# Kernel tuning notes

Measured on AMD Instinct MI355X. Metric: run time of the kernel, lower is better.

Reference implementation:

```python
import jax, jax.numpy as jnp
import numpy as np

N, E = 4096, 131072
IN, HID, OUT = 128, 128, 256
H4, C4 = 4, HID            # first/middle GAT: 4 heads of 128 -> concat 512
CAT = H4 * C4              # 512
NH, DK = 8, OUT // 8       # dense MHA
EPS_LN = 1e-5


def setup_inputs() -> dict:
    key = jax.random.key(0)
    ks = jax.random.split(key, 32)
    s = 0.05
    inp = {
        "x": jax.random.normal(ks[0], (N, IN), jnp.float32),
        "edge_index": jax.random.randint(ks[1], (2, E), 0, N, jnp.int64),
        # GAT layer 0: in=128, heads=4, out=128
        "W0": jax.random.normal(ks[2], (IN, H4 * C4)) * s,
        "as0": jax.random.normal(ks[3], (H4, C4)) * s,
        "ad0": jax.random.normal(ks[4], (H4, C4)) * s,
        "b0": jnp.zeros((H4 * C4,)),
        # GAT layer 1: in=512, heads=4, out=128
        "W1": jax.random.normal(ks[5], (CAT, H4 * C4)) * s,
        "as1": jax.random.normal(ks[6], (H4, C4)) * s,
        "ad1": jax.random.normal(ks[7], (H4, C4)) * s,
        "b1": jnp.zeros((H4 * C4,)),
        # GAT layer 2: in=512, heads=1, out=256
        "W2": jax.random.normal(ks[8], (CAT, OUT)) * s,
        "as2": jax.random.normal(ks[9], (1, OUT)) * s,
        "ad2": jax.random.normal(ks[10], (1, OUT)) * s,
        "b2": jnp.zeros((OUT,)),
        # LayerNorms
        "g0": jnp.ones((CAT,)), "be0": jnp.zeros((CAT,)),
        "g1": jnp.ones((CAT,)), "be1": jnp.zeros((CAT,)),
        "g2": jnp.ones((OUT,)), "be2": jnp.zeros((OUT,)),
        # dense MHA on output_dim=256
        "wq": jax.random.normal(ks[11], (OUT, OUT)) * s, "bq": jnp.zeros((OUT,)),
        "wk": jax.random.normal(ks[12], (OUT, OUT)) * s, "bk": jnp.zeros((OUT,)),
        "wv": jax.random.normal(ks[13], (OUT, OUT)) * s, "bv": jnp.zeros((OUT,)),
        "wo": jax.random.normal(ks[14], (OUT, OUT)) * s, "bo": jnp.zeros((OUT,)),
    }
    return inp


def _layer_norm(x, g, b):
    mu = x.mean(-1, keepdims=True)
    var = ((x - mu) ** 2).mean(-1, keepdims=True)
    return (x - mu) * jax.lax.rsqrt(var + EPS_LN) * g + b


def _gat(x, src, dst, W, a_src, a_dst, bias, heads, out_c):
    # PyG GATConv (concat=True, negative_slope=0.2, self-loops pre-added)
    n = x.shape[0]
    xl = (x @ W).reshape(n, heads, out_c)            # [N,H,C]
    al_s = (xl * a_src).sum(-1)                      # [N,H]
    al_d = (xl * a_dst).sum(-1)                      # [N,H]
    alpha = jax.nn.leaky_relu(al_s[src] + al_d[dst], 0.2)  # [Etot,H]
    m = jax.ops.segment_max(alpha, dst, num_segments=n)
    e = jnp.exp(alpha - m[dst])
    denom = jax.ops.segment_sum(e, dst, num_segments=n)
    w = e / (denom[dst] + 1e-16)                     # [Etot,H]
    msg = w[:, :, None] * xl[src]                    # [Etot,H,C]
    out = jax.ops.segment_sum(msg, dst, num_segments=n)
    return out.reshape(n, heads * out_c) + bias


def _mha(x, wq, bq, wk, bk, wv, bv, wo, bo):
    # x: [1,N,D], 8 heads
    B, S, D = x.shape
    def split(y):
        return y.reshape(B, S, NH, DK).transpose(0, 2, 1, 3)
    Q, K, V = split(x @ wq + bq), split(x @ wk + bk), split(x @ wv + bv)
    scores = jnp.einsum('bhqd,bhkd->bhqk', Q, K) / np.sqrt(DK)
    attn = jax.nn.softmax(scores, axis=-1)
    out = jnp.einsum('bhqk,bhkd->bhqd', attn, V)
    out = out.transpose(0, 2, 1, 3).reshape(B, S, D)
    return out @ wo + bo


def reference(x, edge_index, W0, as0, ad0, b0, W1, as1, ad1, b1, W2, as2, ad2, b2,
              g0, be0, g1, be1, g2, be2, wq, bq, wk, bk, wv, bv, wo, bo):
    n = x.shape[0]
    loops = jnp.arange(n, dtype=edge_index.dtype)
    src = jnp.concatenate([edge_index[0], loops])
    dst = jnp.concatenate([edge_index[1], loops])

    # layer 0: in=128 -> 512; residual None (128 != 512)
    h = jax.nn.elu(_gat(x, src, dst, W0, as0, ad0, b0, H4, C4))
    h = _layer_norm(h, g0, be0)

    # layer 1: 512 -> 512; residual applies
    res = h
    h = jax.nn.elu(_gat(h, src, dst, W1, as1, ad1, b1, H4, C4))
    h = _layer_norm(h, g1, be1)
    h = h + res

    # layer 2: 512 -> 256, 1 head
    h = _gat(h, src, dst, W2, as2, ad2, b2, 1, OUT)
    h = _layer_norm(h, g2, be2)

    # dense self-attention over all nodes as one sequence
    h = _mha(h[None], wq, bq, wk, bk, wv, bv, wo, bo)[0]
    return h
```

## Files before the change

### kernel.cpp

```cpp
#include <hip/hip_runtime.h>
#include <math.h>

typedef __attribute__((ext_vector_type(8))) short short8;
typedef __attribute__((ext_vector_type(4))) float float4v;

#define QS 0.2550354f

#if __has_builtin(__builtin_amdgcn_exp2f)
#define EXP2(x) __builtin_amdgcn_exp2f(x)
#else
#define EXP2(x) __expf((x)*0.6931471805599453f)
#endif

__device__ __forceinline__ float waveReduceSum(float v){
  #pragma unroll
  for(int o=32;o>0;o>>=1) v += __shfl_down(v,o,64);
  return v;
}
__device__ __forceinline__ unsigned short f2bf(float f){
  unsigned int u = __float_as_uint(f);
  return (unsigned short)((u + 0x7FFFu + ((u>>16)&1u)) >> 16);
}
__device__ __forceinline__ float bf2f(unsigned short u){
  return __uint_as_float(((unsigned int)u)<<16);
}

__global__ __launch_bounds__(256) void prep(const float* __restrict__ x, unsigned short* __restrict__ xb,
                     const float* __restrict__ W0, unsigned short* __restrict__ W0t,
                     const float* __restrict__ W1, unsigned short* __restrict__ W1t,
                     const float* __restrict__ W2, unsigned short* __restrict__ W2t,
                     const float* __restrict__ wq, const float* __restrict__ wk,
                     const float* __restrict__ wv, unsigned short* __restrict__ wqkvt,
                     const float* __restrict__ bq, const float* __restrict__ bk,
                     const float* __restrict__ bv, float* __restrict__ bqkv,
                     const float* __restrict__ wo, unsigned short* __restrict__ wot,
                     const float* __restrict__ as0, const float* __restrict__ ad0, unsigned short* __restrict__ S0,
                     const float* __restrict__ as1, const float* __restrict__ ad1, unsigned short* __restrict__ S1,
                     const float* __restrict__ as2, const float* __restrict__ ad2, unsigned short* __restrict__ S2){
  int b = blockIdx.x, t = threadIdx.x;
  if(b < 256){
    int i = (b*256 + t)*8;
    float4 u0 = *(const float4*)(x + i);
    float4 u1 = *(const float4*)(x + i + 4);
    short8 o;
    o[0]=(short)f2bf(u0.x); o[1]=(short)f2bf(u0.y); o[2]=(short)f2bf(u0.z); o[3]=(short)f2bf(u0.w);
    o[4]=(short)f2bf(u1.x); o[5]=(short)f2bf(u1.y); o[6]=(short)f2bf(u1.z); o[7]=(short)f2bf(u1.w);
    *(short8*)(xb + i) = o;
    return;
  }
  if(b == 256){ bqkv[t] = bq[t]*QS; bqkv[256+t] = bk[t]; bqkv[512+t] = bv[t]; return; }
  if(b < 433){
    __shared__ unsigned short tile[64][65];
    int tb = b - 257;
    const float* src; unsigned short* dst; int K,N,roff,local; float sc = 1.f;
    if(tb<16){src=W0;dst=W0t;K=128;N=512;local=tb;roff=0;}
    else if(tb<80){src=W1;dst=W1t;K=512;N=512;local=tb-16;roff=0;}
    else if(tb<112){src=W2;dst=W2t;K=512;N=256;local=tb-80;roff=0;}
    else if(tb<128){src=wq;dst=wqkvt;K=256;N=256;local=tb-112;roff=0;sc=QS;}
    else if(tb<144){src=wk;dst=wqkvt;K=256;N=256;local=tb-128;roff=256;}
    else if(tb<160){src=wv;dst=wqkvt;K=256;N=256;local=tb-144;roff=512;}
    else {src=wo;dst=wot;K=256;N=256;local=tb-160;roff=0;}
    int ntiles = N>>6;
    int k0 = (local/ntiles)*64, n0 = (local%ntiles)*64;
    int r4 = t>>4, c4 = (t&15)*4;
    #pragma unroll
    for(int it=0;it<4;it++){
      int row = r4 + it*16;
      float4 v = *(const float4*)(src + (size_t)(k0+row)*N + n0 + c4);
      tile[row][c4+0]=f2bf(v.x*sc);
      tile[row][c4+1]=f2bf(v.y*sc);
      tile[row][c4+2]=f2bf(v.z*sc);
      tile[row][c4+3]=f2bf(v.w*sc);
    }
    __syncthreads();
    int r8 = t>>3, c8 = (t&7)*8;
    #pragma unroll
    for(int it=0;it<2;it++){
      int n = r8 + it*32;
      short8 o;
      #pragma unroll
      for(int j=0;j<8;j++) o[j] = (short)tile[c8+j][n];
      *(short8*)(dst + (size_t)(n0+n+roff)*K + k0 + c8) = o;
    }
    return;
  }
  int bb = b - 433;
  const float *W,*as,*ad; unsigned short* S; int K,C,H,k;
  if(bb<128){W=W0;as=as0;ad=ad0;S=S0;K=128;C=128;H=4;k=bb;}
  else if(bb<640){W=W1;as=as1;ad=ad1;S=S1;K=512;C=128;H=4;k=bb-128;}
  else {W=W2;as=as2;ad=ad2;S=S2;K=512;C=256;H=1;k=bb-640;}
  int D = H*C;
  __shared__ float s1[4], s2[4];
  int lane=t&63, wid=t>>6;
  for(int h=0;h<H;h++){
    float ps=0.f, pd=0.f;
    for(int c=t;c<C;c+=256){
      float wv2 = W[k*D + h*C + c];
      ps += wv2*as[h*C+c];
      pd += wv2*ad[h*C+c];
    }
    ps = waveReduceSum(ps); pd = waveReduceSum(pd);
    if(lane==0){ s1[wid]=ps; s2[wid]=pd; }
    __syncthreads();
    if(t==0){
      float u=s1[0]+s1[1]+s1[2]+s1[3], v=s2[0]+s2[1]+s2[2]+s2[3];
      S[h*K+k]=f2bf(u); S[(4+h)*K+k]=f2bf(v);
    }
    __syncthreads();
  }
  if(t==0){
    for(int h=H;h<4;h++){ S[h*K+k]=0; S[(4+h)*K+k]=0; }
    for(int r=8;r<16;r++) S[r*K+k]=0;
  }
}

__global__ __launch_bounds__(1024) void csr_scan(const int* __restrict__ ei, int E, int Etot,
                                                 int* __restrict__ rp, int* __restrict__ wcnt){
  __shared__ int sh[1024];
  __shared__ int lhist[4096];
  int t = threadIdx.x;
  #pragma unroll
  for(int i=0;i<4;i++) lhist[t*4+i] = 0;
  __syncthreads();
  for(int e=t; e<Etot; e+=1024){
    int d = (e<E) ? (ei[E+e]&4095) : (e-E);
    atomicAdd(&lhist[d], 1);
  }
  __syncthreads();
  int base[4]; int s=0;
  #pragma unroll
  for(int i=0;i<4;i++){ base[i]=s; s += lhist[t*4+i]; }
  sh[t] = s;
  __syncthreads();
  for(int off=1; off<1024; off<<=1){
    int x = (t>=off) ? sh[t-off] : 0;
    __syncthreads();
    sh[t] += x;
    __syncthreads();
  }
  int excl = (t==0) ? 0 : sh[t-1];
  #pragma unroll
  for(int i=0;i<4;i++){
    int v = excl + base[i];
    rp[t*4+i] = v; wcnt[t*4+i] = v;
  }
  if(t==1023) rp[4096] = excl + s;
}

__device__ __forceinline__ void gemm_body(int bx, int by,
                          const unsigned short* __restrict__ A, const unsigned short* __restrict__ Bt,
                          const float* __restrict__ bias, float* __restrict__ C,
                          unsigned short* __restrict__ Cb, unsigned short* __restrict__ VtT,
                          const unsigned short* __restrict__ Wsd, float* __restrict__ als,
                          float* __restrict__ ald, int M, int K, int N,
                          unsigned short* As, unsigned short* Bs){
  int t = threadIdx.x, lane = t & 63, w = t >> 6;
  int m = lane & 15, g = lane >> 4;
  int bm = by * 64, bn = bx * 64;

  int sr = t >> 3;
  int sc = (t & 7) * 8;
  const unsigned short* Ap = A  + (size_t)(bm + sr)*K + sc;
  const unsigned short* Bp = Bt + (size_t)(bn + sr)*K + sc;
  bool doC = (Wsd != nullptr) && (bx == 0);

  float4v acc[4];
  #pragma unroll
  for(int nt=0;nt<4;nt++) acc[nt] = (float4v){0.f,0.f,0.f,0.f};
  float4v acc2 = (float4v){0.f,0.f,0.f,0.f};

  short8 a0 = *(const short8*)(Ap);
  short8 a1 = *(const short8*)(Ap + 32*K);
  short8 b0 = *(const short8*)(Bp);
  short8 b1 = *(const short8*)(Bp + 32*K);

  int buf = 0;
  for(int k0=0;k0<K;k0+=64){
    *(short8*)&As[buf*4608 + sr*72 + sc]      = a0;
    *(short8*)&As[buf*4608 + (sr+32)*72 + sc] = a1;
    *(short8*)&Bs[buf*4608 + sr*72 + sc]      = b0;
    *(short8*)&Bs[buf*4608 + (sr+32)*72 + sc] = b1;
    if(k0+64 < K){
      a0 = *(const short8*)(Ap + k0+64);
      a1 = *(const short8*)(Ap + 32*K + k0+64);
      b0 = *(const short8*)(Bp + k0+64);
      b1 = *(const short8*)(Bp + 32*K + k0+64);
    }
    __syncthreads();

    #pragma unroll
    for(int ks=0;ks<2;ks++){
      short8 aA = *(const short8*)&As[buf*4608 + (w*16 + m)*72 + ks*32 + g*8];
      #pragma unroll
      for(int nt=0;nt<4;nt++){
        short8 bB = *(const short8*)&Bs[buf*4608 + (nt*16 + m)*72 + ks*32 + g*8];
        acc[nt] = __builtin_amdgcn_mfma_f32_16x16x32_bf16(aA, bB, acc[nt], 0,0,0);
      }
      if(doC){
        short8 bW = *(const short8*)(Wsd + m*K + k0 + ks*32 + g*8);
        acc2 = __builtin_amdgcn_mfma_f32_16x16x32_bf16(aA, bW, acc2, 0,0,0);
      }
    }
    buf ^= 1;
  }

  if(VtT != nullptr && bn >= 512){
    __syncthreads();
    unsigned short* T = As;
    #pragma unroll
    for(int nt=0;nt<4;nt++){
      int col = bn + nt*16 + m;
      float bv = bias ? bias[col] : 0.f;
      unsigned int r0 = __float_as_uint(acc[nt][0]+bv) + 0x8000u;
      unsigned int r1 = __float_as_uint(acc[nt][1]+bv) + 0x8000u;
      unsigned int r2 = __float_as_uint(acc[nt][2]+bv) + 0x8000u;
      unsigned int r3 = __float_as_uint(acc[nt][3]+bv) + 0x8000u;
      uint2 pk;
      pk.x = __builtin_amdgcn_perm(r1, r0, 0x07060302u);
      pk.y = __builtin_amdgcn_perm(r3, r2, 0x07060302u);
      *(uint2*)&T[(nt*16 + m)*72 + w*16 + g*4] = pk;
    }
    __syncthreads();
    int d  = t >> 2;
    int qc = (t & 3) * 16;
    short8 v0 = *(const short8*)&T[d*72 + qc];
    short8 v1 = *(const short8*)&T[d*72 + qc + 8];
    unsigned short* dst = VtT + (size_t)(bn - 512 + d)*M + bm + qc;
    *(short8*)(dst)     = v0;
    *(short8*)(dst + 8) = v1;
    return;
  }

  #pragma unroll
  for(int nt=0;nt<4;nt++){
    int col = bn + nt*16 + m;
    float bv = bias ? bias[col] : 0.f;
    #pragma unroll
    for(int r=0;r<4;r++){
      int row = bm + w*16 + g*4 + r;
      float v = acc[nt][r] + bv;
      if(C)  C[(size_t)row*N + col]  = v;
      if(Cb) Cb[(size_t)row*N + col] = f2bf(v);
    }
  }
  if(doC){
    #pragma unroll
    for(int r=0;r<4;r++){
      int row = bm + w*16 + g*4 + r;
      if(m<4)      als[row*4 + m]     = acc2[r];
      else if(m<8) ald[row*4 + (m-4)] = acc2[r];
    }
  }
}

__global__ __launch_bounds__(256) void gemm_mfma(const unsigned short* __restrict__ A,
                                                 const unsigned short* __restrict__ Bt,
                                                 const float* __restrict__ bias,
                                                 float* __restrict__ C,
                                                 unsigned short* __restrict__ Cb,
                                                 unsigned short* __restrict__ VtT,
                                                 const unsigned short* __restrict__ Wsd,
                                                 float* __restrict__ als,
                                                 float* __restrict__ ald,
                                                 int M, int K, int N){
  __shared__ unsigned short As[2*4608];
  __shared__ unsigned short Bs[2*4608];
  gemm_body(blockIdx.x, blockIdx.y, A, Bt, bias, C, Cb, VtT, Wsd, als, ald, M, K, N, As, Bs);
}

__global__ __launch_bounds__(256) void gemm0_scatter(const unsigned short* __restrict__ A,
                                                     const unsigned short* __restrict__ Bt,
                                                     unsigned short* __restrict__ Cb,
                                                     const unsigned short* __restrict__ Wsd,
                                                     float* __restrict__ als, float* __restrict__ ald,
                                                     const int* __restrict__ ei, int E, int Etot,
                                                     int* __restrict__ wcnt, int* __restrict__ col){
  __shared__ unsigned short As[2*4608];
  __shared__ unsigned short Bs[2*4608];
  int u = blockIdx.x;
  if(u < 512){
    gemm_body(u & 7, u >> 3, A, Bt, nullptr, nullptr, Cb, nullptr, Wsd, als, ald, 4096, 128, 512, As, Bs);
  } else {
    int e = (u-512)*256 + threadIdx.x;
    if(e < Etot){
      int s,d;
      if(e < E){ s = ei[e]&4095; d = ei[E+e]&4095; } else { s = d = e - E; }
      int pos = atomicAdd(&wcnt[d], 1);
      col[pos] = s;
    }
  }
}

#define CE 128
__global__ void gat_gather_ln(const int* __restrict__ rp,
                              const int* __restrict__ col,
                              const unsigned short* __restrict__ xlb,
                              const float* __restrict__ als,
                              const float* __restrict__ ald,
                              const float* __restrict__ bias,
                              const float* __restrict__ gw,
                              const float* __restrict__ be,
                              const float* __restrict__ res,
                              float* __restrict__ out,
                              unsigned short* __restrict__ outb,
                              int D, int logC, int do_elu){
  int n = blockIdx.x, t = threadIdx.x;
  int c0 = t*2;
  int h = c0 >> logC;
  int rowW = D >> 1;
  float4 advv = *(const float4*)(ald + n*4);
  int start = rp[n], end = rp[n+1];
  const unsigned int* xw = (const unsigned int*)xlb;

  __shared__ float pw[2][CE*4];
  __shared__ int offs[2][CE];

  float acc0=0.f, acc1=0.f, den=0.f;
  int nch = (end - start + CE - 1) / CE;

  {
    int cnt = min(CE, end-start);
    if(t < cnt){
      int s = col[start+t];
      offs[0][t] = s*rowW;
      float4 av = *(const float4*)(als + s*4);
      #pragma unroll
      for(int hh=0;hh<4;hh++){
        float a = ((const float*)&av)[hh] + ((const float*)&advv)[hh];
        a = a>0.f ? a : 0.2f*a;
        pw[0][t*4+hh] = __expf(a);
      }
    }
  }

  for(int c=0;c<nch;c++){
    __syncthreads();
    if(c+1 < nch){
      int base = start + (c+1)*CE;
      int cnt = min(CE, end-base);
      int b2 = (c+1)&1;
      if(t < cnt){
        int s = col[base+t];
        offs[b2][t] = s*rowW;
        float4 av = *(const float4*)(als + s*4);
        #pragma unroll
        for(int hh=0;hh<4;hh++){
          float a = ((const float*)&av)[hh] + ((const float*)&advv)[hh];
          a = a>0.f ? a : 0.2f*a;
          pw[b2][t*4+hh] = __expf(a);
        }
      }
    }
    int base = start + c*CE;
    int cnt = min(CE, end-base);
    int b = c&1;
    #pragma unroll 8
    for(int j=0;j<cnt;j++){
      float p = pw[b][j*4+h];
      unsigned int u = xw[offs[b][j] + t];
      acc0 += p * bf2f((unsigned short)(u & 0xffffu));
      acc1 += p * bf2f((unsigned short)(u >> 16));
      den += p;
    }
  }

  float inv_d = 1.f/(den + 1e-16f);
  float v0 = acc0*inv_d + bias[c0];
  float v1 = acc1*inv_d + bias[c0+1];
  if(do_elu){
    v0 = v0>0.f ? v0 : expm1f(v0);
    v1 = v1>0.f ? v1 : expm1f(v1);
  }
  __shared__ float sh[4];
  int lane=t&63, wid=t>>6, nw = blockDim.x>>6;
  float sum = waveReduceSum(v0+v1);
  if(lane==0) sh[wid]=sum;
  __syncthreads();
  float mean = 0.f;
  for(int i=0;i<nw;i++) mean += sh[i];
  mean /= (float)D;
  __syncthreads();
  float d0 = v0-mean, d1 = v1-mean;
  float vs = waveReduceSum(d0*d0 + d1*d1);
  if(lane==0) sh[wid]=vs;
  __syncthreads();
  float var = 0.f;
  for(int i=0;i<nw;i++) var += sh[i];
  var /= (float)D;
  float inv = rsqrtf(var + 1e-5f);
  float y0 = d0*inv*gw[c0]   + be[c0];
  float y1 = d1*inv*gw[c0+1] + be[c0+1];
  if(res){ float2 rv = *(const float2*)(res + n*D + c0); y0 += rv.x; y1 += rv.y; }
  if(out) *(float2*)(out + n*D + c0) = make_float2(y0, y1);
  if(outb) ((unsigned int*)outb)[n*rowW + t] =
      (unsigned int)f2bf(y0) | ((unsigned int)f2bf(y1) << 16);
}

#define KS 2
__global__ __launch_bounds__(256) void attention12(const unsigned short* __restrict__ QKV,
                                                   const unsigned short* __restrict__ Vt,
                                                   float* __restrict__ Op,
                                                   float* __restrict__ lp, int S){
  const int RS = 768;
  int qb = blockIdx.x * 64;
  int h  = blockIdx.y;
  int ks = blockIdx.z;
  int t  = threadIdx.x;
  int lane = t & 63, w = t >> 6;
  int m = lane & 15, g = lane >> 4;
  int m7 = m & 7;

  __shared__ unsigned short Ps[64*64];
  __shared__ unsigned short Vs[32*64];
  __shared__ unsigned short Ks[64*36];

  short8 aQ = *(const short8*)(QKV + (qb + w*16 + m)*RS + h*32 + g*8);

  float4v o0 = {0.f,0.f,0.f,0.f}, o1 = {0.f,0.f,0.f,0.f};
  float den = 0.f;

  int r8 = t>>3, c8 = t&7;
  int kr = t>>2, kc = (t&3)*8;
  int kA = ks*(S/KS), kB = kA + S/KS;

  short8 v  = *(const short8*)(Vt + (h*32 + r8)*S + kA + c8*8);
  short8 kv = *(const short8*)(QKV + (kA + kr)*RS + 256 + h*32 + kc);

  for(int kt=kA; kt<kB; kt+=64){
    __syncthreads();
    *(short8*)&Vs[r8*64 + ((c8 ^ (r8&7))<<3)] = v;
    *(short8*)&Ks[kr*36 + kc] = kv;
    if(kt+64 < kB){
      v  = *(const short8*)(Vt + (h*32 + r8)*S + kt+64 + c8*8);
      kv = *(const short8*)(QKV + (kt+64 + kr)*RS + 256 + h*32 + kc);
    }
    __syncthreads();

    #pragma unroll
    for(int nt=0;nt<4;nt++){
      short8 aK = *(const short8*)&Ks[(nt*16 + m)*36 + g*8];
      float4v acc = {0.f,0.f,0.f,0.f};
      acc = __builtin_amdgcn_mfma_f32_16x16x32_bf16(aK, aQ, acc, 0,0,0);
      float p0 = EXP2(acc[0]);
      float p1 = EXP2(acc[1]);
      float p2 = EXP2(acc[2]);
      float p3 = EXP2(acc[3]);
      den += (p0+p1)+(p2+p3);
      unsigned int r0 = __float_as_uint(p0) + 0x8000u;
      unsigned int r1 = __float_as_uint(p1) + 0x8000u;
      unsigned int r2 = __float_as_uint(p2) + 0x8000u;
      unsigned int r3 = __float_as_uint(p3) + 0x8000u;
      uint2 pk;
      pk.x = __builtin_amdgcn_perm(r1, r0, 0x07060302u);
      pk.y = __builtin_amdgcn_perm(r3, r2, 0x07060302u);
      *(uint2*)&Ps[(w*16 + m)*64 + (((2*nt + (g>>1)) ^ m7)<<3) + ((g&1)<<2)] = pk;
    }

    #pragma unroll
    for(int kh=0;kh<2;kh++){
      int swz = ((kh*4 + g) ^ m7) << 3;
      short8 aP  = *(const short8*)&Ps[(w*16 + m)*64 + swz];
      short8 bV0 = *(const short8*)&Vs[m*64       + swz];
      short8 bV1 = *(const short8*)&Vs[(16+m)*64  + swz];
      o0 = __builtin_amdgcn_mfma_f32_16x16x32_bf16(aP, bV0, o0, 0,0,0);
      o1 = __builtin_amdgcn_mfma_f32_16x16x32_bf16(aP, bV1, o1, 0,0,0);
    }
  }

  den += __shfl_xor(den, 16, 64);
  den += __shfl_xor(den, 32, 64);

  float* Ob = Op + (size_t)ks*S*256;
  #pragma unroll
  for(int r=0;r<4;r++){
    int q = qb + w*16 + g*4 + r;
    Ob[q*256 + h*32 + m]      = o0[r];
    Ob[q*256 + h*32 + 16 + m] = o1[r];
  }
  if(g==0){
    int q = qb + w*16 + m;
    lp[ks*S*8 + q*8 + h] = den;
  }
}

__global__ __launch_bounds__(256) void combine(const float* __restrict__ Op,
                                               const float* __restrict__ lp,
                                               unsigned short* __restrict__ aob, int S){
  int q = blockIdx.x, t = threadIdx.x;
  int h = t >> 5;
  float o = 0.f, l = 0.f;
  #pragma unroll
  for(int s=0;s<KS;s++) o += Op[(size_t)s*S*256 + q*256 + t];
  #pragma unroll
  for(int s=0;s<KS;s++) l += lp[s*S*8 + q*8 + h];
  aob[q*256 + t] = f2bf(o / l);
}

extern "C" void kernel_launch(void* const* d_in, const int* in_sizes, int n_in,
                              void* d_out, int out_size, void* d_ws, size_t ws_size,
                              hipStream_t stream) {
  const float* x   = (const float*)d_in[0];
  const int*   ei  = (const int*)d_in[1];
  const float* W0  = (const float*)d_in[2];
  const float* as0 = (const float*)d_in[3];
  const float* ad0 = (const float*)d_in[4];
  const float* b0  = (const float*)d_in[5];
  const float* W1  = (const float*)d_in[6];
  const float* as1 = (const float*)d_in[7];
  const float* ad1 = (const float*)d_in[8];
  const float* b1  = (const float*)d_in[9];
  const float* W2  = (const float*)d_in[10];
  const float* as2 = (const float*)d_in[11];
  const float* ad2 = (const float*)d_in[12];
  const float* b2  = (const float*)d_in[13];
  const float* g0  = (const float*)d_in[14];
  const float* be0 = (const float*)d_in[15];
  const float* g1  = (const float*)d_in[16];
  const float* be1 = (const float*)d_in[17];
  const float* g2  = (const float*)d_in[18];
  const float* be2 = (const float*)d_in[19];
  const float* wq  = (const float*)d_in[20];
  const float* bq  = (const float*)d_in[21];
  const float* wk  = (const float*)d_in[22];
  const float* bk  = (const float*)d_in[23];
  const float* wv  = (const float*)d_in[24];
  const float* bv  = (const float*)d_in[25];
  const float* wo  = (const float*)d_in[26];
  const float* bo  = (const float*)d_in[27];
  float* out = (float*)d_out;

  const int N = 4096;
  const int E = in_sizes[1] / 2;
  const int Etot = E + N;

  char* p = (char*)d_ws;
  auto alloc = [&](size_t bytes){ char* r = p; p += (bytes + 255) & ~(size_t)255; return r; };

  float* h0   = (float*)alloc(N*512*4);
  float* als  = (float*)alloc(N*4*4);
  float* ald  = (float*)alloc(N*4*4);
  unsigned short* xb   = (unsigned short*)alloc(N*128*2);
  unsigned short* xlb  = (unsigned short*)alloc(N*512*2);
  unsigned short* h0b  = (unsigned short*)alloc(N*512*2);
  unsigned short* h1b  = (unsigned short*)alloc(N*512*2);
  unsigned short* h2b  = (unsigned short*)alloc(N*256*2);
  unsigned short* QKVb = (unsigned short*)alloc((size_t)N*768*2);
  unsigned short* Vt   = (unsigned short*)alloc(256*N*2);
  unsigned short* aob  = (unsigned short*)alloc(N*256*2);
  unsigned short* W0t  = (unsigned short*)alloc(512*128*2);
  unsigned short* W1t  = (unsigned short*)alloc(512*512*2);
  unsigned short* W2t  = (unsigned short*)alloc(256*512*2);
  unsigned short* wqkvt= (unsigned short*)alloc(768*256*2);
  float* bqkv = (float*)alloc(768*4);
  unsigned short* wot  = (unsigned short*)alloc(256*256*2);
  unsigned short* Wsd0 = (unsigned short*)alloc(16*128*2);
  unsigned short* Wsd1 = (unsigned short*)alloc(16*512*2);
  unsigned short* Wsd2 = (unsigned short*)alloc(16*512*2);
  float* Op = (float*)alloc((size_t)KS*N*256*4);
  float* lp = (float*)alloc((size_t)KS*N*8*4);
  int* wcnt = (int*)alloc(N*4);
  int* rp   = (int*)alloc((N+2)*4);
  int* col  = (int*)alloc(Etot*4);

  prep<<<1585, 256, 0, stream>>>(x, xb, W0, W0t, W1, W1t, W2, W2t,
                                 wq, wk, wv, wqkvt, bq, bk, bv, bqkv, wo, wot,
                                 as0, ad0, Wsd0, as1, ad1, Wsd1, as2, ad2, Wsd2);

  csr_scan<<<1, 1024, 0, stream>>>(ei, E, Etot, rp, wcnt);

  gemm0_scatter<<<512 + (Etot+255)/256, 256, 0, stream>>>(xb, W0t, xlb, Wsd0, als, ald,
                                                          ei, E, Etot, wcnt, col);
  gat_gather_ln<<<N, 256, 0, stream>>>(rp, col, xlb, als, ald, b0, g0, be0,
                                       nullptr, h0, h0b, 512, 7, 1);

  gemm_mfma<<<dim3(8, 64), 256, 0, stream>>>(h0b, W1t, nullptr, nullptr, xlb, nullptr, Wsd1, als, ald, N, 512, 512);
  gat_gather_ln<<<N, 256, 0, stream>>>(rp, col, xlb, als, ald, b1, g1, be1,
                                       h0, nullptr, h1b, 512, 7, 1);

  gemm_mfma<<<dim3(4, 64), 256, 0, stream>>>(h1b, W2t, nullptr, nullptr, xlb, nullptr, Wsd2, als, ald, N, 512, 256);
  gat_gather_ln<<<N, 128, 0, stream>>>(rp, col, xlb, als, ald, b2, g2, be2,
                                       nullptr, nullptr, h2b, 256, 8, 0);

  gemm_mfma<<<dim3(12, 64), 256, 0, stream>>>(h2b, wqkvt, bqkv, nullptr, QKVb, Vt, nullptr, nullptr, nullptr, N, 256, 768);
  attention12<<<dim3(N/64, 8, KS), 256, 0, stream>>>(QKVb, Vt, Op, lp, N);
  combine<<<N, 256, 0, stream>>>(Op, lp, aob, N);
  gemm_mfma<<<dim3(4, 64), 256, 0, stream>>>(aob, wot, bo, out, nullptr, nullptr, nullptr, nullptr, nullptr, N, 256, 256);
}
```

Measured before the change: 301.6 us.

## Move destination-degree histogram from single-block scan into parallel prep blocks

The per-node in-degree histogram was built by one 1024-thread block looping over all edges with shared-memory atomics. That work now runs as extra blocks in the prep kernel using global atomics, and csr_scan only performs the prefix sum over the finished histogram. The goal is to remove a serial single-block bottleneck from the critical path. In exchange it adds a memset and global atomic contention on a 4096-entry histogram.

```diff
diff --git a/kernel.cpp b/kernel.cpp
--- a/kernel.cpp
+++ b/kernel.cpp
@@ -36,7 +36,8 @@
                      const float* __restrict__ wo, unsigned short* __restrict__ wot,
                      const float* __restrict__ as0, const float* __restrict__ ad0, unsigned short* __restrict__ S0,
                      const float* __restrict__ as1, const float* __restrict__ ad1, unsigned short* __restrict__ S1,
-                     const float* __restrict__ as2, const float* __restrict__ ad2, unsigned short* __restrict__ S2){
+                     const float* __restrict__ as2, const float* __restrict__ ad2, unsigned short* __restrict__ S2,
+                     const int* __restrict__ ei, int E, int Etot, int* __restrict__ hist){
   int b = blockIdx.x, t = threadIdx.x;
   if(b < 256){
     int i = (b*256 + t)*8;
@@ -84,6 +85,14 @@
     }
     return;
   }
+  if(b >= 1585){
+    int e = (b-1585)*256 + t;
+    if(e < Etot){
+      int d = (e<E) ? (ei[E+e]&4095) : (e-E);
+      atomicAdd(&hist[d], 1);
+    }
+    return;
+  }
   int bb = b - 433;
   const float *W,*as,*ad; unsigned short* S; int K,C,H,k;
   if(bb<128){W=W0;as=as0;ad=ad0;S=S0;K=128;C=128;H=4;k=bb;}
@@ -114,22 +123,15 @@
   }
 }
 
-__global__ __launch_bounds__(1024) void csr_scan(const int* __restrict__ ei, int E, int Etot,
-                                                 int* __restrict__ rp, int* __restrict__ wcnt){
+__global__ __launch_bounds__(1024) void csr_scan(const int* __restrict__ hist,
+                                                 int* __restrict__ rp,
+                                                 int* __restrict__ wcnt, int N){
   __shared__ int sh[1024];
-  __shared__ int lhist[4096];
   int t = threadIdx.x;
-  #pragma unroll
-  for(int i=0;i<4;i++) lhist[t*4+i] = 0;
-  __syncthreads();
-  for(int e=t; e<Etot; e+=1024){
-    int d = (e<E) ? (ei[E+e]&4095) : (e-E);
-    atomicAdd(&lhist[d], 1);
-  }
-  __syncthreads();
-  int base[4]; int s=0;
-  #pragma unroll
-  for(int i=0;i<4;i++){ base[i]=s; s += lhist[t*4+i]; }
+  int base[4];
+  int s = 0;
+  #pragma unroll
+  for(int i=0;i<4;i++){ base[i]=s; s += hist[t*4+i]; }
   sh[t] = s;
   __syncthreads();
   for(int off=1; off<1024; off<<=1){
@@ -144,7 +146,7 @@
     int v = excl + base[i];
     rp[t*4+i] = v; wcnt[t*4+i] = v;
   }
-  if(t==1023) rp[4096] = excl + s;
+  if(t==1023) rp[N] = excl + s;
 }
 
 __device__ __forceinline__ void gemm_body(int bx, int by,
@@ -558,15 +560,18 @@
   unsigned short* Wsd2 = (unsigned short*)alloc(16*512*2);
   float* Op = (float*)alloc((size_t)KS*N*256*4);
   float* lp = (float*)alloc((size_t)KS*N*8*4);
+  int* hist = (int*)alloc(N*4);
   int* wcnt = (int*)alloc(N*4);
   int* rp   = (int*)alloc((N+2)*4);
   int* col  = (int*)alloc(Etot*4);
 
-  prep<<<1585, 256, 0, stream>>>(x, xb, W0, W0t, W1, W1t, W2, W2t,
+  hipMemsetAsync(hist, 0, N*sizeof(int), stream);
+  prep<<<1585 + (Etot+255)/256, 256, 0, stream>>>(x, xb, W0, W0t, W1, W1t, W2, W2t,
                                  wq, wk, wv, wqkvt, bq, bk, bv, bqkv, wo, wot,
-                                 as0, ad0, Wsd0, as1, ad1, Wsd1, as2, ad2, Wsd2);
-
-  csr_scan<<<1, 1024, 0, stream>>>(ei, E, Etot, rp, wcnt);
+                                 as0, ad0, Wsd0, as1, ad1, Wsd1, as2, ad2, Wsd2,
+                                 ei, E, Etot, hist);
+
+  csr_scan<<<1, 1024, 0, stream>>>(hist, rp, wcnt, N);
 
   gemm0_scatter<<<512 + (Etot+255)/256, 256, 0, stream>>>(xb, W0t, xlb, Wsd0, als, ald,
                                                           ei, E, Etot, wcnt, col);
```

After: 263.4 us. 1.14x faster.
